# Kernel tuning notes

Hardware: AMD Instinct MI355X
Metric: run time of the kernel (lower is better)

## Reference

```python
import jax, jax.numpy as jnp
import numpy as np

N = 100_000          # nodes
E = 3_200_000        # edges (avg degree 32)
DIMS = [6, 20, 15, 10, 5, 2]


def setup_inputs() -> dict:
    key = jax.random.key(0)
    ks = jax.random.split(key, 3 + 2 * 5)
    inp = {
        "x": jax.random.normal(ks[0], (N, DIMS[0]), jnp.float32),
        "edge_index": jax.random.randint(ks[1], (2, E), 0, N, jnp.int32),
        "edge_weight": jax.random.uniform(ks[2], (E,), jnp.float32),
    }
    for i in range(5):
        din, dout = DIMS[i], DIMS[i + 1]
        s = 1.0 / np.sqrt(din)
        inp[f"w_rel{i}"] = jax.random.normal(ks[3 + 2 * i], (din, dout), jnp.float32) * s
        inp[f"b_rel{i}"] = jnp.zeros((dout,), jnp.float32)
        inp[f"w_root{i}"] = jax.random.normal(ks[4 + 2 * i], (din, dout), jnp.float32) * s
    return inp


def _graph_conv(x, src, dst, w, W_rel, b_rel, W_root):
    # PyG GraphConv: lin_rel(scatter_add(w_e * x_src)) + lin_root(x)
    msg = x[src] * w[:, None]                                  # [E, din]
    agg = jax.ops.segment_sum(msg, dst, num_segments=N)        # [N, din]
    return agg @ W_rel + b_rel + x @ W_root                    # [N, dout]


def reference(x, edge_index, edge_weight,
              w_rel0, b_rel0, w_root0,
              w_rel1, b_rel1, w_root1,
              w_rel2, b_rel2, w_root2,
              w_rel3, b_rel3, w_root3,
              w_rel4, b_rel4, w_root4):
    src, dst = edge_index[0], edge_index[1]
    layers = [
        (w_rel0, b_rel0, w_root0),
        (w_rel1, b_rel1, w_root1),
        (w_rel2, b_rel2, w_root2),
        (w_rel3, b_rel3, w_root3),
        (w_rel4, b_rel4, w_root4),
    ]
    for W_rel, b_rel, W_root in layers:
        x = jax.nn.relu(_graph_conv(x, src, dst, edge_weight, W_rel, b_rel, W_root))
    return jax.nn.softmax(x, axis=1)
```

## Files before the change

kernel.cpp:

```cpp
#include <hip/hip_runtime.h>
#include <hip/hip_fp16.h>
#include <stdint.h>

#define N_NODES 100000
#define N_EDGES 3200000
#define BN      64
#define NB      1563
#define NCH_H   1024
#define CH_H    (N_EDGES / NCH_H)
#define CPL     (NCH_H / 64)
#define PAD_PER 98
#define NCH_S   256
#define CH_S    (N_EDGES / NCH_S)
#define BS1     1024
#define S1_IT   ((CH_S + BS1 - 1) / BS1)
#define S2_CAP  2560
#define BLOCK   256
#define W_SCALE 32767.0f
#define W_INV   (1.0f / 32767.0f)

__global__ void hist_kernel(const int* __restrict__ dst, int* __restrict__ hist_g,
                            const float* __restrict__ x, __half* __restrict__ xpad) {
    __shared__ int h[NB];
    for (int b = threadIdx.x; b < NB; b += BLOCK) h[b] = 0;
    {
        int i = blockIdx.x * PAD_PER + threadIdx.x;
        if (threadIdx.x < PAD_PER && i < N_NODES) {
            const float* xr = x + (size_t)i * 6;
            __half2 hh[4];
            hh[0] = __halves2half2(__float2half(xr[0]), __float2half(xr[1]));
            hh[1] = __halves2half2(__float2half(xr[2]), __float2half(xr[3]));
            hh[2] = __halves2half2(__float2half(xr[4]), __float2half(xr[5]));
            hh[3] = __halves2half2(__float2half(0.f),   __float2half(0.f));
            *(uint4*)(xpad + (size_t)i * 8) = *(uint4*)hh;
        }
    }
    __syncthreads();
    const int c  = blockIdx.x;
    const int k0 = c * CH_H;
    for (int k = threadIdx.x; k < CH_H; k += BLOCK)
        atomicAdd(&h[dst[k0 + k] >> 6], 1);
    __syncthreads();
    for (int b = threadIdx.x; b < NB; b += BLOCK)
        hist_g[c * NB + b] = h[b];
}

__global__ void chunkscan_kernel(const int* __restrict__ hist_g,
                                 int* __restrict__ off_g, int* __restrict__ tot) {
    int w    = (blockIdx.x * blockDim.x + threadIdx.x) >> 6;
    int lane = threadIdx.x & 63;
    if (w >= NB) return;
    int v[CPL];
    int ls = 0;
    const int cbase = lane * CPL;
    #pragma unroll
    for (int i = 0; i < CPL; ++i) { v[i] = hist_g[(cbase + i) * NB + w]; ls += v[i]; }
    int run = ls;
    #pragma unroll
    for (int d = 1; d < 64; d <<= 1) {
        int u = __shfl_up(run, d);
        if (lane >= d) run += u;
    }
    int acc = run - ls;
    #pragma unroll
    for (int i = 0; i < CPL; ++i) { off_g[(cbase + i) * NB + w] = acc; acc += v[i]; }
    if (lane == 63) tot[w] = acc;
}

#define SCAN_T   1024
#define SCAN_PER 2
__global__ void scan_kernel(const int* __restrict__ cnt, int* __restrict__ bstart) {
    __shared__ int part[SCAN_T];
    int t = threadIdx.x;
    int local[SCAN_PER];
    int s = 0;
    #pragma unroll
    for (int i = 0; i < SCAN_PER; ++i) {
        int idx = t * SCAN_PER + i;
        int v = (idx < NB) ? cnt[idx] : 0;
        local[i] = s;
        s += v;
    }
    part[t] = s;
    __syncthreads();
    for (int off = 1; off < SCAN_T; off <<= 1) {
        int v = (t >= off) ? part[t - off] : 0;
        __syncthreads();
        part[t] += v;
        __syncthreads();
    }
    int excl = part[t] - s;
    #pragma unroll
    for (int i = 0; i < SCAN_PER; ++i) {
        int idx = t * SCAN_PER + i;
        if (idx < NB) bstart[idx] = excl + local[i];
    }
}

__global__ void __launch_bounds__(BS1)
scatter1_kernel(const int* __restrict__ src, const int* __restrict__ dst,
                const float* __restrict__ w,
                const int* __restrict__ bstart, const int* __restrict__ off_g,
                uint2* __restrict__ rec1) {
    __shared__ uint32_t stage[CH_S];
    __shared__ int h[NB];
    __shared__ int delta[NB];
    __shared__ int wtot[BS1 / 64];

    const int c  = blockIdx.x;
    const int k0 = c * CH_S;
    const int t  = threadIdx.x;

    for (int b = t; b < NB; b += BS1) h[b] = 0;
    __syncthreads();
    int dstv[S1_IT];
    int nit = 0;
    for (int k = t; k < CH_S; k += BS1, ++nit) {
        int d = dst[k0 + k];
        dstv[nit] = d;
        atomicAdd(&h[d >> 6], 1);
    }
    __syncthreads();

    {
        const int base = t * 2;
        int v[2], ls = 0;
        #pragma unroll
        for (int i = 0; i < 2; ++i) {
            int idx = base + i;
            v[i] = (idx < NB) ? h[idx] : 0;
            ls += v[i];
        }
        int lane = t & 63, wv = t >> 6;
        int run = ls;
        #pragma unroll
        for (int d = 1; d < 64; d <<= 1) {
            int u = __shfl_up(run, d);
            if (lane >= d) run += u;
        }
        if (lane == 63) wtot[wv] = run;
        __syncthreads();
        int wexcl = 0;
        for (int i = 0; i < wv; ++i) wexcl += wtot[i];
        int excl = wexcl + run - ls;
        #pragma unroll
        for (int i = 0; i < 2; ++i) {
            int idx = base + i;
            if (idx < NB) {
                int gb = bstart[idx] + off_g[(size_t)(4 * c) * NB + idx];
                h[idx]     = excl;
                delta[idx] = gb - excl;
                excl += v[i];
            }
        }
    }
    __syncthreads();

    nit = 0;
    for (int k = t; k < CH_S; k += BS1, ++nit) {
        int d = dstv[nit];
        int b = d >> 6;
        int pos = atomicAdd(&h[b], 1);
        stage[pos] = (uint32_t)k | ((uint32_t)(d & 63) << 14) | ((uint32_t)b << 20);
    }
    __syncthreads();

    for (int i = t; i < CH_S; i += BS1) {
        uint32_t sv = stage[i];
        int le = sv & 0x3FFF;
        int dl = (sv >> 14) & 0x3F;
        int b  = sv >> 20;
        int e  = k0 + le;
        uint2 r;
        r.x = (uint32_t)src[e] | ((uint32_t)dl << 17);
        r.y = __float_as_uint(w[e]);
        rec1[delta[b] + i] = r;
    }
}

__global__ void scatter2_kernel(const uint2* __restrict__ rec1,
                                const int* __restrict__ bstart, const int* __restrict__ tot,
                                uint32_t* __restrict__ rec2,
                                int* __restrict__ row_start, int* __restrict__ cnt) {
    __shared__ int h[BN];
    __shared__ int cur[BN];
    __shared__ uint32_t stage[S2_CAP];
    const int b  = blockIdx.x;
    const int s0 = bstart[b];
    const int n  = tot[b];
    if (threadIdx.x < BN) h[threadIdx.x] = 0;
    __syncthreads();
    for (int k = threadIdx.x; k < n; k += BLOCK)
        atomicAdd(&h[rec1[s0 + k].x >> 17], 1);
    __syncthreads();
    if (threadIdx.x < BN) {
        int v = h[threadIdx.x];
        int run = v;
        #pragma unroll
        for (int d = 1; d < 64; d <<= 1) {
            int u = __shfl_up(run, d);
            if (threadIdx.x >= d) run += u;
        }
        int excl = run - v;
        cur[threadIdx.x] = excl;
        int node = b * BN + threadIdx.x;
        if (node < N_NODES) { row_start[node] = s0 + excl; cnt[node] = v; }
    }
    __syncthreads();
    for (int k = threadIdx.x; k < n; k += BLOCK) {
        uint2 r = rec1[s0 + k];
        int dl = (int)(r.x >> 17);
        float wv = __uint_as_float(r.y);
        uint32_t w15 = (uint32_t)__float2uint_rn(wv * W_SCALE);
        uint32_t r2 = (r.x & 0x1FFFF) | (w15 << 17);
        int pos = atomicAdd(&cur[dl], 1);
        if (pos < S2_CAP) stage[pos] = r2;
        else              rec2[s0 + pos] = r2;
    }
    __syncthreads();
    for (int i = threadIdx.x; i < n && i < S2_CAP; i += BLOCK)
        rec2[s0 + i] = stage[i];
}

__global__ void layer0_kernel(const __half* __restrict__ xpad,
                              const uint32_t* __restrict__ rec,
                              const int* __restrict__ row_start, const int* __restrict__ cnt,
                              const float* __restrict__ wrel0, const float* __restrict__ brel0,
                              const float* __restrict__ wroot0,
                              const float* __restrict__ wrel1, const float* __restrict__ brel1,
                              const float* __restrict__ wroot1,
                              __half* __restrict__ pn, float* __restrict__ oinitn) {
    __shared__ float s_wrel0[6 * 20], s_wroot0[6 * 20], s_b0[20];
    __shared__ float s_wrel1[20 * 15], s_wroot1[20 * 15], s_b1[15];
    for (int t = threadIdx.x; t < 120; t += BLOCK) {
        s_wrel0[t]  = wrel0[t];
        s_wroot0[t] = wroot0[t];
    }
    for (int t = threadIdx.x; t < 300; t += BLOCK) {
        s_wrel1[t]  = wrel1[t];
        s_wroot1[t] = wroot1[t];
    }
    if (threadIdx.x < 20) s_b0[threadIdx.x] = brel0[threadIdx.x];
    if (threadIdx.x < 15) s_b1[threadIdx.x] = brel1[threadIdx.x];
    __syncthreads();

    int t = blockIdx.x * blockDim.x + threadIdx.x;
    int node = t >> 3;
    int q    = t & 7;

    float agg[6] = {0.f, 0.f, 0.f, 0.f, 0.f, 0.f};
    const int s = row_start[node];
    const int e = s + cnt[node];
    for (int k = s + q; k < e; k += 32) {
        uint32_t rv[4];
        float    wv[4];
        #pragma unroll
        for (int u = 0; u < 4; ++u) {
            int kk = k + 8 * u;
            int kc = kk < e ? kk : (e - 1);
            rv[u] = rec[kc];
            wv[u] = kk < e ? (float)(rv[u] >> 17) * W_INV : 0.f;
        }
        uint4 raw[4];
        #pragma unroll
        for (int u = 0; u < 4; ++u)
            raw[u] = *(const uint4*)(xpad + (size_t)(rv[u] & 0x1FFFF) * 8);
        #pragma unroll
        for (int u = 0; u < 4; ++u) {
            const __half2* h = (const __half2*)&raw[u];
            float w = wv[u];
            agg[0] += w * __low2float(h[0]);  agg[1] += w * __high2float(h[0]);
            agg[2] += w * __low2float(h[1]);  agg[3] += w * __high2float(h[1]);
            agg[4] += w * __low2float(h[2]);  agg[5] += w * __high2float(h[2]);
        }
    }
    #pragma unroll
    for (int i = 0; i < 6; ++i) {
        agg[i] += __shfl_xor(agg[i], 1);
        agg[i] += __shfl_xor(agg[i], 2);
        agg[i] += __shfl_xor(agg[i], 4);
    }
    uint4 raws = *(const uint4*)(xpad + (size_t)node * 8);
    const __half2* hs = (const __half2*)&raws;
    float xv[6] = { __low2float(hs[0]), __high2float(hs[0]),
                    __low2float(hs[1]), __high2float(hs[1]),
                    __low2float(hs[2]), __high2float(hs[2]) };

    float ov[20];
    #pragma unroll
    for (int j = 0; j < 20; ++j) {
        float o = s_b0[j];
        #pragma unroll
        for (int i = 0; i < 6; ++i)
            o += agg[i] * s_wrel0[i * 20 + j] + xv[i] * s_wroot0[i * 20 + j];
        ov[j] = fmaxf(o, 0.f);
    }

    {
        float pk[2] = {0.f, 0.f};
        #pragma unroll
        for (int kk = 0; kk < 2; ++kk) {
            int k = 2 * q + kk;
            if (k < 15) {
                float sacc = 0.f;
                #pragma unroll
                for (int j = 0; j < 20; ++j) sacc += ov[j] * s_wrel1[j * 15 + k];
                pk[kk] = sacc;
            }
        }
        ((__half2*)(pn + (size_t)node * 16))[q] =
            __halves2half2(__float2half(pk[0]), __float2half(pk[1]));
    }
    #pragma unroll
    for (int kk = 0; kk < 2; ++kk) {
        int k = q + kk * 8;
        if (k < 15) {
            float sacc = s_b1[k];
            #pragma unroll
            for (int j = 0; j < 20; ++j) sacc += ov[j] * s_wroot1[j * 15 + k];
            oinitn[(size_t)node * 15 + k] = sacc;
        }
    }
}

template<int DOUT, int SPH, int NDOUT, int NSPH, bool LAST>
__global__ void gather_kernel(const __half* __restrict__ p, const float* __restrict__ oinit,
                              const uint32_t* __restrict__ rec,
                              const int* __restrict__ row_start, const int* __restrict__ cnt,
                              const float* __restrict__ wrel_n, const float* __restrict__ brel_n,
                              const float* __restrict__ wroot_n,
                              __half* __restrict__ pn, float* __restrict__ oinitn,
                              float* __restrict__ out) {
    __shared__ float s_wrel[LAST ? 1 : DOUT * NDOUT];
    __shared__ float s_wroot[LAST ? 1 : DOUT * NDOUT];
    __shared__ float s_b[LAST ? 1 : (NDOUT > 0 ? NDOUT : 1)];
    if constexpr (!LAST) {
        for (int t = threadIdx.x; t < DOUT * NDOUT; t += BLOCK) {
            s_wrel[t]  = wrel_n[t];
            s_wroot[t] = wroot_n[t];
        }
        if (threadIdx.x < NDOUT) s_b[threadIdx.x] = brel_n[threadIdx.x];
        __syncthreads();
    }

    int t = blockIdx.x * blockDim.x + threadIdx.x;
    int node = t >> 3;
    int q    = t & 7;

    float af[SPH];
    #pragma unroll
    for (int i = 0; i < SPH; ++i) af[i] = 0.f;

    const int s = row_start[node];
    const int e = s + cnt[node];
    constexpr int NR = (SPH >= 8) ? SPH / 8 : 1;
    for (int k = s + q; k < e; k += 32) {
        uint32_t rv[4];
        float    wv[4];
        #pragma unroll
        for (int u = 0; u < 4; ++u) {
            int kk = k + 8 * u;
            int kc = kk < e ? kk : (e - 1);
            rv[u] = rec[kc];
            wv[u] = kk < e ? (float)(rv[u] >> 17) * W_INV : 0.f;
        }
        if constexpr (SPH >= 8) {
            uint4 raw[4 * NR];
            #pragma unroll
            for (int u = 0; u < 4; ++u) {
                const uint4* ps = (const uint4*)(p + (size_t)(rv[u] & 0x1FFFF) * SPH);
                #pragma unroll
                for (int v = 0; v < NR; ++v) raw[u * NR + v] = ps[v];
            }
            #pragma unroll
            for (int u = 0; u < 4; ++u) {
                float w = wv[u];
                #pragma unroll
                for (int v = 0; v < NR; ++v) {
                    const __half2* h = (const __half2*)&raw[u * NR + v];
                    #pragma unroll
                    for (int jj = 0; jj < 4; ++jj) {
                        af[v * 8 + 2 * jj]     += w * __low2float(h[jj]);
                        af[v * 8 + 2 * jj + 1] += w * __high2float(h[jj]);
                    }
                }
            }
        } else {
            uint32_t raw[4];
            #pragma unroll
            for (int u = 0; u < 4; ++u)
                raw[u] = *(const uint32_t*)(p + (size_t)(rv[u] & 0x1FFFF) * SPH);
            #pragma unroll
            for (int u = 0; u < 4; ++u) {
                __half2 h = *(const __half2*)&raw[u];
                af[0] += wv[u] * __low2float(h);
                af[1] += wv[u] * __high2float(h);
            }
        }
    }
    #pragma unroll
    for (int i = 0; i < SPH; ++i) {
        af[i] += __shfl_xor(af[i], 1);
        af[i] += __shfl_xor(af[i], 2);
        af[i] += __shfl_xor(af[i], 4);
    }

    if constexpr (LAST) {
        if (q == 0) {
            float o0 = af[0] + oinit[(size_t)node * 2 + 0];
            float o1 = af[1] + oinit[(size_t)node * 2 + 1];
            float m = fmaxf(o0, o1);
            float e0 = __expf(o0 - m), e1 = __expf(o1 - m);
            float inv = 1.f / (e0 + e1);
            out[(size_t)node * 2 + 0] = e0 * inv;
            out[(size_t)node * 2 + 1] = e1 * inv;
        }
    } else {
        float ov[DOUT];
        #pragma unroll
        for (int j = 0; j < DOUT; ++j)
            ov[j] = fmaxf(af[j] + oinit[(size_t)node * DOUT + j], 0.f);

        if (q < NSPH / 2) {
            float pk[2] = {0.f, 0.f};
            #pragma unroll
            for (int kk = 0; kk < 2; ++kk) {
                int k = 2 * q + kk;
                if (k < NDOUT) {
                    float sacc = 0.f;
                    #pragma unroll
                    for (int j = 0; j < DOUT; ++j) sacc += ov[j] * s_wrel[j * NDOUT + k];
                    pk[kk] = sacc;
                }
            }
            ((__half2*)(pn + (size_t)node * NSPH))[q] =
                __halves2half2(__float2half(pk[0]), __float2half(pk[1]));
        }
        #pragma unroll
        for (int kk = 0; kk < 2; ++kk) {
            int k = q + kk * 8;
            if (k < NDOUT) {
                float sacc = s_b[k];
                #pragma unroll
                for (int j = 0; j < DOUT; ++j) sacc += ov[j] * s_wroot[j * NDOUT + k];
                oinitn[(size_t)node * NDOUT + k] = sacc;
            }
        }
    }
}


extern "C" void kernel_launch(void* const* d_in, const int* in_sizes, int n_in,
                              void* d_out, int out_size, void* d_ws, size_t ws_size,
                              hipStream_t stream) {
    const float* x  = (const float*)d_in[0];
    const int*   ei = (const int*)d_in[1];
    const float* ew = (const float*)d_in[2];
    const float* wrel[5]  = { (const float*)d_in[3], (const float*)d_in[6],
                              (const float*)d_in[9], (const float*)d_in[12],
                              (const float*)d_in[15] };
    const float* brel[5]  = { (const float*)d_in[4], (const float*)d_in[7],
                              (const float*)d_in[10], (const float*)d_in[13],
                              (const float*)d_in[16] };
    const float* wroot[5] = { (const float*)d_in[5], (const float*)d_in[8],
                              (const float*)d_in[11], (const float*)d_in[14],
                              (const float*)d_in[17] };

    char* ws = (char*)d_ws;
    size_t off = 0;
    auto alloc = [&](size_t bytes) -> void* {
        void* ptr = ws + off;
        off += (bytes + 255) & ~(size_t)255;
        return ptr;
    };
    char*     regionA   = (char*)alloc((size_t)N_EDGES * 8);
    uint2*    rec1      = (uint2*)regionA;
    __half*   pA        = (__half*)regionA;
    __half*   pB        = (__half*)(regionA + (size_t)4  * 1024 * 1024);
    float*    oA        = (float*)(regionA + (size_t)8  * 1024 * 1024);
    float*    oB        = (float*)(regionA + (size_t)16 * 1024 * 1024);
    uint32_t* rec2      = (uint32_t*)alloc((size_t)N_EDGES * 4);
    __half*   xpad      = (__half*)alloc((size_t)N_NODES * 8 * 2);
    int*      hist_g    = (int*)alloc((size_t)NCH_H * NB * 4);
    int*      off_g     = (int*)alloc((size_t)NCH_H * NB * 4);
    int*      tot       = (int*)alloc((size_t)NB * 4);
    int*      bstart    = (int*)alloc((size_t)NB * 4);
    int*      row_start = (int*)alloc((size_t)N_NODES * 4);
    int*      cntb      = (int*)alloc((size_t)N_NODES * 4);

    const int* srcv = ei;
    const int* dstv = ei + N_EDGES;

    const int gN8 = (8 * N_NODES + BLOCK - 1) / BLOCK;

    hist_kernel     <<<NCH_H, BLOCK, 0, stream>>>(dstv, hist_g, x, xpad);
    chunkscan_kernel<<<(NB + 3) / 4, BLOCK, 0, stream>>>(hist_g, off_g, tot);
    scan_kernel     <<<1, SCAN_T, 0, stream>>>(tot, bstart);
    scatter1_kernel <<<NCH_S, BS1, 0, stream>>>(srcv, dstv, ew, bstart, off_g, rec1);
    scatter2_kernel <<<NB, BLOCK, 0, stream>>>(rec1, bstart, tot, rec2, row_start, cntb);

    layer0_kernel<<<gN8, BLOCK, 0, stream>>>(xpad, rec2, row_start, cntb,
                                             wrel[0], brel[0], wroot[0],
                                             wrel[1], brel[1], wroot[1], pA, oA);
    gather_kernel<15, 16, 10, 16, false><<<gN8, BLOCK, 0, stream>>>(
        pA, oA, rec2, row_start, cntb, wrel[2], brel[2], wroot[2], pB, oB, nullptr);
    gather_kernel<10, 16, 5, 8, false><<<gN8, BLOCK, 0, stream>>>(
        pB, oB, rec2, row_start, cntb, wrel[3], brel[3], wroot[3], pA, oA, nullptr);
    gather_kernel<5, 8, 2, 2, false><<<gN8, BLOCK, 0, stream>>>(
        pA, oA, rec2, row_start, cntb, wrel[4], brel[4], wroot[4], pB, oB, nullptr);
    gather_kernel<2, 2, 0, 0, true><<<gN8, BLOCK, 0, stream>>>(
        pB, oB, rec2, row_start, cntb, nullptr, nullptr, nullptr,
        nullptr, nullptr, (float*)d_out);
}
```

Measured before the change: 322.7 us.

## Fuse five layer kernels into one persistent kernel with grid barriers

```diff
diff --git a/kernel.cpp b/kernel.cpp
--- a/kernel.cpp
+++ b/kernel.cpp
@@ -16,6 +16,7 @@
 #define S1_IT   ((CH_S + BS1 - 1) / BS1)
 #define S2_CAP  2560
 #define BLOCK   256
+#define PGRID   512
 #define W_SCALE 32767.0f
 #define W_INV   (1.0f / 32767.0f)
 
@@ -222,231 +223,286 @@
         rec2[s0 + i] = stage[i];
 }
 
-__global__ void layer0_kernel(const __half* __restrict__ xpad,
-                              const uint32_t* __restrict__ rec,
-                              const int* __restrict__ row_start, const int* __restrict__ cnt,
-                              const float* __restrict__ wrel0, const float* __restrict__ brel0,
-                              const float* __restrict__ wroot0,
-                              const float* __restrict__ wrel1, const float* __restrict__ brel1,
-                              const float* __restrict__ wroot1,
-                              __half* __restrict__ pn, float* __restrict__ oinitn) {
-    __shared__ float s_wrel0[6 * 20], s_wroot0[6 * 20], s_b0[20];
-    __shared__ float s_wrel1[20 * 15], s_wroot1[20 * 15], s_b1[15];
-    for (int t = threadIdx.x; t < 120; t += BLOCK) {
-        s_wrel0[t]  = wrel0[t];
-        s_wroot0[t] = wroot0[t];
-    }
-    for (int t = threadIdx.x; t < 300; t += BLOCK) {
-        s_wrel1[t]  = wrel1[t];
-        s_wroot1[t] = wroot1[t];
-    }
-    if (threadIdx.x < 20) s_b0[threadIdx.x] = brel0[threadIdx.x];
-    if (threadIdx.x < 15) s_b1[threadIdx.x] = brel1[threadIdx.x];
-    __syncthreads();
-
-    int t = blockIdx.x * blockDim.x + threadIdx.x;
-    int node = t >> 3;
-    int q    = t & 7;
-
-    float agg[6] = {0.f, 0.f, 0.f, 0.f, 0.f, 0.f};
-    const int s = row_start[node];
-    const int e = s + cnt[node];
-    for (int k = s + q; k < e; k += 32) {
-        uint32_t rv[4];
-        float    wv[4];
-        #pragma unroll
-        for (int u = 0; u < 4; ++u) {
-            int kk = k + 8 * u;
-            int kc = kk < e ? kk : (e - 1);
-            rv[u] = rec[kc];
-            wv[u] = kk < e ? (float)(rv[u] >> 17) * W_INV : 0.f;
-        }
-        uint4 raw[4];
-        #pragma unroll
-        for (int u = 0; u < 4; ++u)
-            raw[u] = *(const uint4*)(xpad + (size_t)(rv[u] & 0x1FFFF) * 8);
-        #pragma unroll
-        for (int u = 0; u < 4; ++u) {
-            const __half2* h = (const __half2*)&raw[u];
-            float w = wv[u];
-            agg[0] += w * __low2float(h[0]);  agg[1] += w * __high2float(h[0]);
-            agg[2] += w * __low2float(h[1]);  agg[3] += w * __high2float(h[1]);
-            agg[4] += w * __low2float(h[2]);  agg[5] += w * __high2float(h[2]);
-        }
-    }
-    #pragma unroll
-    for (int i = 0; i < 6; ++i) {
-        agg[i] += __shfl_xor(agg[i], 1);
-        agg[i] += __shfl_xor(agg[i], 2);
-        agg[i] += __shfl_xor(agg[i], 4);
-    }
-    uint4 raws = *(const uint4*)(xpad + (size_t)node * 8);
-    const __half2* hs = (const __half2*)&raws;
-    float xv[6] = { __low2float(hs[0]), __high2float(hs[0]),
-                    __low2float(hs[1]), __high2float(hs[1]),
-                    __low2float(hs[2]), __high2float(hs[2]) };
-
-    float ov[20];
-    #pragma unroll
-    for (int j = 0; j < 20; ++j) {
-        float o = s_b0[j];
-        #pragma unroll
-        for (int i = 0; i < 6; ++i)
-            o += agg[i] * s_wrel0[i * 20 + j] + xv[i] * s_wroot0[i * 20 + j];
-        ov[j] = fmaxf(o, 0.f);
-    }
-
-    {
-        float pk[2] = {0.f, 0.f};
-        #pragma unroll
-        for (int kk = 0; kk < 2; ++kk) {
-            int k = 2 * q + kk;
-            if (k < 15) {
-                float sacc = 0.f;
+__device__ __forceinline__ void grid_barrier(int* bar, int* local_sense) {
+    __threadfence();
+    __syncthreads();
+    if (threadIdx.x == 0) {
+        int want = *local_sense ^ 1;
+        *local_sense = want;
+        int arrived = __hip_atomic_fetch_add(&bar[0], 1, __ATOMIC_ACQ_REL,
+                                             __HIP_MEMORY_SCOPE_AGENT);
+        if (arrived == PGRID - 1) {
+            __hip_atomic_store(&bar[0], 0, __ATOMIC_RELAXED, __HIP_MEMORY_SCOPE_AGENT);
+            __hip_atomic_store(&bar[1], want, __ATOMIC_RELEASE, __HIP_MEMORY_SCOPE_AGENT);
+        } else {
+            while (__hip_atomic_load(&bar[1], __ATOMIC_ACQUIRE,
+                                     __HIP_MEMORY_SCOPE_AGENT) != want) {}
+        }
+    }
+    __syncthreads();
+    __threadfence();
+}
+
+struct LayerArgs {
+    const __half* xpad;
+    const uint32_t* rec;
+    const int* row_start;
+    const int* cnt;
+    const float* wrel[5];
+    const float* brel[5];
+    const float* wroot[5];
+    __half* pA; __half* pB;
+    float*  oA; float*  oB;
+    float*  out;
+    int*    bar;
+};
+
+template<int DOUT, int SPH, int NDOUT, int NSPH, bool LAST>
+__device__ __forceinline__ void gather_body(
+        const __half* __restrict__ p, const float* __restrict__ oinit,
+        const uint32_t* __restrict__ rec,
+        const int* __restrict__ row_start, const int* __restrict__ cnt,
+        const float* s_wrel, const float* s_wroot, const float* s_b,
+        __half* __restrict__ pn, float* __restrict__ oinitn,
+        float* __restrict__ out, int gtid, int NT) {
+    for (int t = gtid; t < 8 * N_NODES; t += NT) {
+        int node = t >> 3;
+        int q    = t & 7;
+
+        float af[SPH];
+        #pragma unroll
+        for (int i = 0; i < SPH; ++i) af[i] = 0.f;
+
+        const int s = row_start[node];
+        const int e = s + cnt[node];
+        constexpr int NR = (SPH >= 8) ? SPH / 8 : 1;
+        for (int k = s + q; k < e; k += 32) {
+            uint32_t rv[4];
+            float    wv[4];
+            #pragma unroll
+            for (int u = 0; u < 4; ++u) {
+                int kk = k + 8 * u;
+                int kc = kk < e ? kk : (e - 1);
+                rv[u] = rec[kc];
+                wv[u] = kk < e ? (float)(rv[u] >> 17) * W_INV : 0.f;
+            }
+            if constexpr (SPH >= 8) {
+                uint4 raw[4 * NR];
                 #pragma unroll
-                for (int j = 0; j < 20; ++j) sacc += ov[j] * s_wrel1[j * 15 + k];
-                pk[kk] = sacc;
-            }
-        }
-        ((__half2*)(pn + (size_t)node * 16))[q] =
-            __halves2half2(__float2half(pk[0]), __float2half(pk[1]));
-    }
-    #pragma unroll
-    for (int kk = 0; kk < 2; ++kk) {
-        int k = q + kk * 8;
-        if (k < 15) {
-            float sacc = s_b1[k];
-            #pragma unroll
-            for (int j = 0; j < 20; ++j) sacc += ov[j] * s_wroot1[j * 15 + k];
-            oinitn[(size_t)node * 15 + k] = sacc;
-        }
-    }
-}
-
-template<int DOUT, int SPH, int NDOUT, int NSPH, bool LAST>
-__global__ void gather_kernel(const __half* __restrict__ p, const float* __restrict__ oinit,
-                              const uint32_t* __restrict__ rec,
-                              const int* __restrict__ row_start, const int* __restrict__ cnt,
-                              const float* __restrict__ wrel_n, const float* __restrict__ brel_n,
-                              const float* __restrict__ wroot_n,
-                              __half* __restrict__ pn, float* __restrict__ oinitn,
-                              float* __restrict__ out) {
-    __shared__ float s_wrel[LAST ? 1 : DOUT * NDOUT];
-    __shared__ float s_wroot[LAST ? 1 : DOUT * NDOUT];
-    __shared__ float s_b[LAST ? 1 : (NDOUT > 0 ? NDOUT : 1)];
-    if constexpr (!LAST) {
-        for (int t = threadIdx.x; t < DOUT * NDOUT; t += BLOCK) {
-            s_wrel[t]  = wrel_n[t];
-            s_wroot[t] = wroot_n[t];
-        }
-        if (threadIdx.x < NDOUT) s_b[threadIdx.x] = brel_n[threadIdx.x];
-        __syncthreads();
-    }
-
-    int t = blockIdx.x * blockDim.x + threadIdx.x;
-    int node = t >> 3;
-    int q    = t & 7;
-
-    float af[SPH];
-    #pragma unroll
-    for (int i = 0; i < SPH; ++i) af[i] = 0.f;
-
-    const int s = row_start[node];
-    const int e = s + cnt[node];
-    constexpr int NR = (SPH >= 8) ? SPH / 8 : 1;
-    for (int k = s + q; k < e; k += 32) {
-        uint32_t rv[4];
-        float    wv[4];
-        #pragma unroll
-        for (int u = 0; u < 4; ++u) {
-            int kk = k + 8 * u;
-            int kc = kk < e ? kk : (e - 1);
-            rv[u] = rec[kc];
-            wv[u] = kk < e ? (float)(rv[u] >> 17) * W_INV : 0.f;
-        }
-        if constexpr (SPH >= 8) {
-            uint4 raw[4 * NR];
-            #pragma unroll
-            for (int u = 0; u < 4; ++u) {
-                const uint4* ps = (const uint4*)(p + (size_t)(rv[u] & 0x1FFFF) * SPH);
+                for (int u = 0; u < 4; ++u) {
+                    const uint4* ps = (const uint4*)(p + (size_t)(rv[u] & 0x1FFFF) * SPH);
+                    #pragma unroll
+                    for (int v = 0; v < NR; ++v) raw[u * NR + v] = ps[v];
+                }
                 #pragma unroll
-                for (int v = 0; v < NR; ++v) raw[u * NR + v] = ps[v];
-            }
-            #pragma unroll
-            for (int u = 0; u < 4; ++u) {
-                float w = wv[u];
-                #pragma unroll
-                for (int v = 0; v < NR; ++v) {
-                    const __half2* h = (const __half2*)&raw[u * NR + v];
+                for (int u = 0; u < 4; ++u) {
+                    float w = wv[u];
                     #pragma unroll
-                    for (int jj = 0; jj < 4; ++jj) {
-                        af[v * 8 + 2 * jj]     += w * __low2float(h[jj]);
-                        af[v * 8 + 2 * jj + 1] += w * __high2float(h[jj]);
+                    for (int v = 0; v < NR; ++v) {
+                        const __half2* h = (const __half2*)&raw[u * NR + v];
+                        #pragma unroll
+                        for (int jj = 0; jj < 4; ++jj) {
+                            af[v * 8 + 2 * jj]     += w * __low2float(h[jj]);
+                            af[v * 8 + 2 * jj + 1] += w * __high2float(h[jj]);
+                        }
                     }
                 }
+            } else {
+                uint32_t raw[4];
+                #pragma unroll
+                for (int u = 0; u < 4; ++u)
+                    raw[u] = *(const uint32_t*)(p + (size_t)(rv[u] & 0x1FFFF) * SPH);
+                #pragma unroll
+                for (int u = 0; u < 4; ++u) {
+                    __half2 h = *(const __half2*)&raw[u];
+                    af[0] += wv[u] * __low2float(h);
+                    af[1] += wv[u] * __high2float(h);
+                }
+            }
+        }
+        #pragma unroll
+        for (int i = 0; i < SPH; ++i) {
+            af[i] += __shfl_xor(af[i], 1);
+            af[i] += __shfl_xor(af[i], 2);
+            af[i] += __shfl_xor(af[i], 4);
+        }
+
+        if constexpr (LAST) {
+            if (q == 0) {
+                float o0 = af[0] + oinit[(size_t)node * 2 + 0];
+                float o1 = af[1] + oinit[(size_t)node * 2 + 1];
+                float m = fmaxf(o0, o1);
+                float e0 = __expf(o0 - m), e1 = __expf(o1 - m);
+                float inv = 1.f / (e0 + e1);
+                out[(size_t)node * 2 + 0] = e0 * inv;
+                out[(size_t)node * 2 + 1] = e1 * inv;
             }
         } else {
-            uint32_t raw[4];
+            float ov[DOUT];
+            #pragma unroll
+            for (int j = 0; j < DOUT; ++j)
+                ov[j] = fmaxf(af[j] + oinit[(size_t)node * DOUT + j], 0.f);
+
+            if (q < NSPH / 2) {
+                float pk[2] = {0.f, 0.f};
+                #pragma unroll
+                for (int kk = 0; kk < 2; ++kk) {
+                    int k = 2 * q + kk;
+                    if (k < NDOUT) {
+                        float sacc = 0.f;
+                        #pragma unroll
+                        for (int j = 0; j < DOUT; ++j) sacc += ov[j] * s_wrel[j * NDOUT + k];
+                        pk[kk] = sacc;
+                    }
+                }
+                ((__half2*)(pn + (size_t)node * NSPH))[q] =
+                    __halves2half2(__float2half(pk[0]), __float2half(pk[1]));
+            }
+            #pragma unroll
+            for (int kk = 0; kk < 2; ++kk) {
+                int k = q + kk * 8;
+                if (k < NDOUT) {
+                    float sacc = s_b[k];
+                    #pragma unroll
+                    for (int j = 0; j < DOUT; ++j) sacc += ov[j] * s_wroot[j * NDOUT + k];
+                    oinitn[(size_t)node * NDOUT + k] = sacc;
+                }
+            }
+        }
+    }
+}
+
+__global__ void __launch_bounds__(BLOCK, 2)
+layers_kernel(LayerArgs a) {
+    __shared__ float s_wrel0[6 * 20], s_wroot0[6 * 20], s_b0[20];
+    __shared__ float s_wrel[20 * 15], s_wroot[20 * 15], s_b[16];
+
+    const int gtid = blockIdx.x * blockDim.x + threadIdx.x;
+    const int NT   = gridDim.x * blockDim.x;
+    int sense = 0;
+
+    for (int t = threadIdx.x; t < 120; t += BLOCK) {
+        s_wrel0[t]  = a.wrel[0][t];
+        s_wroot0[t] = a.wroot[0][t];
+    }
+    for (int t = threadIdx.x; t < 300; t += BLOCK) {
+        s_wrel[t]  = a.wrel[1][t];
+        s_wroot[t] = a.wroot[1][t];
+    }
+    if (threadIdx.x < 20) s_b0[threadIdx.x] = a.brel[0][threadIdx.x];
+    if (threadIdx.x < 15) s_b[threadIdx.x]  = a.brel[1][threadIdx.x];
+    __syncthreads();
+
+    for (int t = gtid; t < 8 * N_NODES; t += NT) {
+        int node = t >> 3;
+        int q    = t & 7;
+        float agg[6] = {0.f, 0.f, 0.f, 0.f, 0.f, 0.f};
+        const int s = a.row_start[node];
+        const int e = s + a.cnt[node];
+        for (int k = s + q; k < e; k += 32) {
+            uint32_t rv[4];
+            float    wv[4];
+            #pragma unroll
+            for (int u = 0; u < 4; ++u) {
+                int kk = k + 8 * u;
+                int kc = kk < e ? kk : (e - 1);
+                rv[u] = a.rec[kc];
+                wv[u] = kk < e ? (float)(rv[u] >> 17) * W_INV : 0.f;
+            }
+            uint4 raw[4];
             #pragma unroll
             for (int u = 0; u < 4; ++u)
-                raw[u] = *(const uint32_t*)(p + (size_t)(rv[u] & 0x1FFFF) * SPH);
+                raw[u] = *(const uint4*)(a.xpad + (size_t)(rv[u] & 0x1FFFF) * 8);
             #pragma unroll
             for (int u = 0; u < 4; ++u) {
-                __half2 h = *(const __half2*)&raw[u];
-                af[0] += wv[u] * __low2float(h);
-                af[1] += wv[u] * __high2float(h);
-            }
-        }
-    }
-    #pragma unroll
-    for (int i = 0; i < SPH; ++i) {
-        af[i] += __shfl_xor(af[i], 1);
-        af[i] += __shfl_xor(af[i], 2);
-        af[i] += __shfl_xor(af[i], 4);
-    }
-
-    if constexpr (LAST) {
-        if (q == 0) {
-            float o0 = af[0] + oinit[(size_t)node * 2 + 0];
-            float o1 = af[1] + oinit[(size_t)node * 2 + 1];
-            float m = fmaxf(o0, o1);
-            float e0 = __expf(o0 - m), e1 = __expf(o1 - m);
-            float inv = 1.f / (e0 + e1);
-            out[(size_t)node * 2 + 0] = e0 * inv;
-            out[(size_t)node * 2 + 1] = e1 * inv;
-        }
-    } else {
-        float ov[DOUT];
-        #pragma unroll
-        for (int j = 0; j < DOUT; ++j)
-            ov[j] = fmaxf(af[j] + oinit[(size_t)node * DOUT + j], 0.f);
-
-        if (q < NSPH / 2) {
+                const __half2* h = (const __half2*)&raw[u];
+                float w = wv[u];
+                agg[0] += w * __low2float(h[0]);  agg[1] += w * __high2float(h[0]);
+                agg[2] += w * __low2float(h[1]);  agg[3] += w * __high2float(h[1]);
+                agg[4] += w * __low2float(h[2]);  agg[5] += w * __high2float(h[2]);
+            }
+        }
+        #pragma unroll
+        for (int i = 0; i < 6; ++i) {
+            agg[i] += __shfl_xor(agg[i], 1);
+            agg[i] += __shfl_xor(agg[i], 2);
+            agg[i] += __shfl_xor(agg[i], 4);
+        }
+        uint4 raws = *(const uint4*)(a.xpad + (size_t)node * 8);
+        const __half2* hs = (const __half2*)&raws;
+        float xv[6] = { __low2float(hs[0]), __high2float(hs[0]),
+                        __low2float(hs[1]), __high2float(hs[1]),
+                        __low2float(hs[2]), __high2float(hs[2]) };
+        float ov[20];
+        #pragma unroll
+        for (int j = 0; j < 20; ++j) {
+            float o = s_b0[j];
+            #pragma unroll
+            for (int i = 0; i < 6; ++i)
+                o += agg[i] * s_wrel0[i * 20 + j] + xv[i] * s_wroot0[i * 20 + j];
+            ov[j] = fmaxf(o, 0.f);
+        }
+        {
             float pk[2] = {0.f, 0.f};
             #pragma unroll
             for (int kk = 0; kk < 2; ++kk) {
                 int k = 2 * q + kk;
-                if (k < NDOUT) {
+                if (k < 15) {
                     float sacc = 0.f;
                     #pragma unroll
-                    for (int j = 0; j < DOUT; ++j) sacc += ov[j] * s_wrel[j * NDOUT + k];
+                    for (int j = 0; j < 20; ++j) sacc += ov[j] * s_wrel[j * 15 + k];
                     pk[kk] = sacc;
                 }
             }
-            ((__half2*)(pn + (size_t)node * NSPH))[q] =
+            ((__half2*)(a.pA + (size_t)node * 16))[q] =
                 __halves2half2(__float2half(pk[0]), __float2half(pk[1]));
         }
         #pragma unroll
         for (int kk = 0; kk < 2; ++kk) {
             int k = q + kk * 8;
-            if (k < NDOUT) {
+            if (k < 15) {
                 float sacc = s_b[k];
                 #pragma unroll
-                for (int j = 0; j < DOUT; ++j) sacc += ov[j] * s_wroot[j * NDOUT + k];
-                oinitn[(size_t)node * NDOUT + k] = sacc;
-            }
-        }
-    }
+                for (int j = 0; j < 20; ++j) sacc += ov[j] * s_wroot[j * 15 + k];
+                a.oA[(size_t)node * 15 + k] = sacc;
+            }
+        }
+    }
+    grid_barrier(a.bar, &sense);
+
+    for (int t = threadIdx.x; t < 150; t += BLOCK) {
+        s_wrel[t]  = a.wrel[2][t];
+        s_wroot[t] = a.wroot[2][t];
+    }
+    if (threadIdx.x < 10) s_b[threadIdx.x] = a.brel[2][threadIdx.x];
+    __syncthreads();
+    gather_body<15, 16, 10, 16, false>(a.pA, a.oA, a.rec, a.row_start, a.cnt,
+                                       s_wrel, s_wroot, s_b, a.pB, a.oB, nullptr, gtid, NT);
+    grid_barrier(a.bar, &sense);
+
+    for (int t = threadIdx.x; t < 50; t += BLOCK) {
+        s_wrel[t]  = a.wrel[3][t];
+        s_wroot[t] = a.wroot[3][t];
+    }
+    if (threadIdx.x < 5) s_b[threadIdx.x] = a.brel[3][threadIdx.x];
+    __syncthreads();
+    gather_body<10, 16, 5, 8, false>(a.pB, a.oB, a.rec, a.row_start, a.cnt,
+                                     s_wrel, s_wroot, s_b, a.pA, a.oA, nullptr, gtid, NT);
+    grid_barrier(a.bar, &sense);
+
+    for (int t = threadIdx.x; t < 10; t += BLOCK) {
+        s_wrel[t]  = a.wrel[4][t];
+        s_wroot[t] = a.wroot[4][t];
+    }
+    if (threadIdx.x < 2) s_b[threadIdx.x] = a.brel[4][threadIdx.x];
+    __syncthreads();
+    gather_body<5, 8, 2, 2, false>(a.pA, a.oA, a.rec, a.row_start, a.cnt,
+                                   s_wrel, s_wroot, s_b, a.pB, a.oB, nullptr, gtid, NT);
+    grid_barrier(a.bar, &sense);
+
+    gather_body<2, 2, 0, 0, true>(a.pB, a.oB, a.rec, a.row_start, a.cnt,
+                                  nullptr, nullptr, nullptr,
+                                  nullptr, nullptr, a.out, gtid, NT);
 }
 
 
@@ -456,15 +512,6 @@
     const float* x  = (const float*)d_in[0];
     const int*   ei = (const int*)d_in[1];
     const float* ew = (const float*)d_in[2];
-    const float* wrel[5]  = { (const float*)d_in[3], (const float*)d_in[6],
-                              (const float*)d_in[9], (const float*)d_in[12],
-                              (const float*)d_in[15] };
-    const float* brel[5]  = { (const float*)d_in[4], (const float*)d_in[7],
-                              (const float*)d_in[10], (const float*)d_in[13],
-                              (const float*)d_in[16] };
-    const float* wroot[5] = { (const float*)d_in[5], (const float*)d_in[8],
-                              (const float*)d_in[11], (const float*)d_in[14],
-                              (const float*)d_in[17] };
 
     char* ws = (char*)d_ws;
     size_t off = 0;
@@ -487,11 +534,12 @@
     int*      bstart    = (int*)alloc((size_t)NB * 4);
     int*      row_start = (int*)alloc((size_t)N_NODES * 4);
     int*      cntb      = (int*)alloc((size_t)N_NODES * 4);
+    int*      bar       = (int*)alloc(256);
 
     const int* srcv = ei;
     const int* dstv = ei + N_EDGES;
 
-    const int gN8 = (8 * N_NODES + BLOCK - 1) / BLOCK;
+    hipMemsetAsync(bar, 0, 8, stream);
 
     hist_kernel     <<<NCH_H, BLOCK, 0, stream>>>(dstv, hist_g, x, xpad);
     chunkscan_kernel<<<(NB + 3) / 4, BLOCK, 0, stream>>>(hist_g, off_g, tot);
@@ -499,16 +547,15 @@
     scatter1_kernel <<<NCH_S, BS1, 0, stream>>>(srcv, dstv, ew, bstart, off_g, rec1);
     scatter2_kernel <<<NB, BLOCK, 0, stream>>>(rec1, bstart, tot, rec2, row_start, cntb);
 
-    layer0_kernel<<<gN8, BLOCK, 0, stream>>>(xpad, rec2, row_start, cntb,
-                                             wrel[0], brel[0], wroot[0],
-                                             wrel[1], brel[1], wroot[1], pA, oA);
-    gather_kernel<15, 16, 10, 16, false><<<gN8, BLOCK, 0, stream>>>(
-        pA, oA, rec2, row_start, cntb, wrel[2], brel[2], wroot[2], pB, oB, nullptr);
-    gather_kernel<10, 16, 5, 8, false><<<gN8, BLOCK, 0, stream>>>(
-        pB, oB, rec2, row_start, cntb, wrel[3], brel[3], wroot[3], pA, oA, nullptr);
-    gather_kernel<5, 8, 2, 2, false><<<gN8, BLOCK, 0, stream>>>(
-        pA, oA, rec2, row_start, cntb, wrel[4], brel[4], wroot[4], pB, oB, nullptr);
-    gather_kernel<2, 2, 0, 0, true><<<gN8, BLOCK, 0, stream>>>(
-        pB, oB, rec2, row_start, cntb, nullptr, nullptr, nullptr,
-        nullptr, nullptr, (float*)d_out);
-}
+    LayerArgs la;
+    la.xpad = xpad; la.rec = rec2; la.row_start = row_start; la.cnt = cntb;
+    for (int i = 0; i < 5; ++i) {
+        la.wrel[i]  = (const float*)d_in[3 + 3 * i];
+        la.brel[i]  = (const float*)d_in[4 + 3 * i];
+        la.wroot[i] = (const float*)d_in[5 + 3 * i];
+    }
+    la.pA = pA; la.pB = pB; la.oA = oA; la.oB = oB; la.out = (float*)d_out;
+    la.bar = bar;
+
+    layers_kernel<<<PGRID, BLOCK, 0, stream>>>(la);
+}
```

New measurement: 997.6 us. 3.09x slower.

## Use 16 lanes per node in gather kernels and cache rec1 in shared memory

Applied to the files above, without the earlier changes.

```diff
diff --git a/kernel.cpp b/kernel.cpp
--- a/kernel.cpp
+++ b/kernel.cpp
@@ -16,6 +16,7 @@
 #define S1_IT   ((CH_S + BS1 - 1) / BS1)
 #define S2_CAP  2560
 #define BLOCK   256
+#define LPN     16
 #define W_SCALE 32767.0f
 #define W_INV   (1.0f / 32767.0f)
 
@@ -184,14 +185,18 @@
                                 int* __restrict__ row_start, int* __restrict__ cnt) {
     __shared__ int h[BN];
     __shared__ int cur[BN];
-    __shared__ uint32_t stage[S2_CAP];
+    __shared__ uint2 sin[S2_CAP];
+    __shared__ uint32_t sout[S2_CAP];
     const int b  = blockIdx.x;
     const int s0 = bstart[b];
     const int n  = tot[b];
     if (threadIdx.x < BN) h[threadIdx.x] = 0;
     __syncthreads();
-    for (int k = threadIdx.x; k < n; k += BLOCK)
-        atomicAdd(&h[rec1[s0 + k].x >> 17], 1);
+    for (int k = threadIdx.x; k < n; k += BLOCK) {
+        uint2 r = rec1[s0 + k];
+        if (k < S2_CAP) sin[k] = r;
+        atomicAdd(&h[r.x >> 17], 1);
+    }
     __syncthreads();
     if (threadIdx.x < BN) {
         int v = h[threadIdx.x];
@@ -208,18 +213,18 @@
     }
     __syncthreads();
     for (int k = threadIdx.x; k < n; k += BLOCK) {
-        uint2 r = rec1[s0 + k];
+        uint2 r = (k < S2_CAP) ? sin[k] : rec1[s0 + k];
         int dl = (int)(r.x >> 17);
         float wv = __uint_as_float(r.y);
         uint32_t w15 = (uint32_t)__float2uint_rn(wv * W_SCALE);
         uint32_t r2 = (r.x & 0x1FFFF) | (w15 << 17);
         int pos = atomicAdd(&cur[dl], 1);
-        if (pos < S2_CAP) stage[pos] = r2;
+        if (pos < S2_CAP) sout[pos] = r2;
         else              rec2[s0 + pos] = r2;
     }
     __syncthreads();
     for (int i = threadIdx.x; i < n && i < S2_CAP; i += BLOCK)
-        rec2[s0 + i] = stage[i];
+        rec2[s0 + i] = sout[i];
 }
 
 __global__ void layer0_kernel(const __half* __restrict__ xpad,
@@ -245,28 +250,28 @@
     __syncthreads();
 
     int t = blockIdx.x * blockDim.x + threadIdx.x;
-    int node = t >> 3;
-    int q    = t & 7;
+    int node = t >> 4;
+    int q    = t & 15;
 
     float agg[6] = {0.f, 0.f, 0.f, 0.f, 0.f, 0.f};
     const int s = row_start[node];
     const int e = s + cnt[node];
-    for (int k = s + q; k < e; k += 32) {
-        uint32_t rv[4];
-        float    wv[4];
-        #pragma unroll
-        for (int u = 0; u < 4; ++u) {
-            int kk = k + 8 * u;
+    for (int k = s + q; k < e; k += 2 * LPN) {
+        uint32_t rv[2];
+        float    wv[2];
+        #pragma unroll
+        for (int u = 0; u < 2; ++u) {
+            int kk = k + LPN * u;
             int kc = kk < e ? kk : (e - 1);
             rv[u] = rec[kc];
             wv[u] = kk < e ? (float)(rv[u] >> 17) * W_INV : 0.f;
         }
-        uint4 raw[4];
-        #pragma unroll
-        for (int u = 0; u < 4; ++u)
+        uint4 raw[2];
+        #pragma unroll
+        for (int u = 0; u < 2; ++u)
             raw[u] = *(const uint4*)(xpad + (size_t)(rv[u] & 0x1FFFF) * 8);
         #pragma unroll
-        for (int u = 0; u < 4; ++u) {
+        for (int u = 0; u < 2; ++u) {
             const __half2* h = (const __half2*)&raw[u];
             float w = wv[u];
             agg[0] += w * __low2float(h[0]);  agg[1] += w * __high2float(h[0]);
@@ -279,13 +284,13 @@
         agg[i] += __shfl_xor(agg[i], 1);
         agg[i] += __shfl_xor(agg[i], 2);
         agg[i] += __shfl_xor(agg[i], 4);
+        agg[i] += __shfl_xor(agg[i], 8);
     }
     uint4 raws = *(const uint4*)(xpad + (size_t)node * 8);
     const __half2* hs = (const __half2*)&raws;
     float xv[6] = { __low2float(hs[0]), __high2float(hs[0]),
                     __low2float(hs[1]), __high2float(hs[1]),
                     __low2float(hs[2]), __high2float(hs[2]) };
-
     float ov[20];
     #pragma unroll
     for (int j = 0; j < 20; ++j) {
@@ -295,8 +300,7 @@
             o += agg[i] * s_wrel0[i * 20 + j] + xv[i] * s_wroot0[i * 20 + j];
         ov[j] = fmaxf(o, 0.f);
     }
-
-    {
+    if (q < 8) {
         float pk[2] = {0.f, 0.f};
         #pragma unroll
         for (int kk = 0; kk < 2; ++kk) {
@@ -311,15 +315,11 @@
         ((__half2*)(pn + (size_t)node * 16))[q] =
             __halves2half2(__float2half(pk[0]), __float2half(pk[1]));
     }
-    #pragma unroll
-    for (int kk = 0; kk < 2; ++kk) {
-        int k = q + kk * 8;
-        if (k < 15) {
-            float sacc = s_b1[k];
-            #pragma unroll
-            for (int j = 0; j < 20; ++j) sacc += ov[j] * s_wroot1[j * 15 + k];
-            oinitn[(size_t)node * 15 + k] = sacc;
-        }
+    if (q < 15) {
+        float sacc = s_b1[q];
+        #pragma unroll
+        for (int j = 0; j < 20; ++j) sacc += ov[j] * s_wroot1[j * 15 + q];
+        oinitn[(size_t)node * 15 + q] = sacc;
     }
 }
 
@@ -344,8 +344,8 @@
     }
 
     int t = blockIdx.x * blockDim.x + threadIdx.x;
-    int node = t >> 3;
-    int q    = t & 7;
+    int node = t >> 4;
+    int q    = t & 15;
 
     float af[SPH];
     #pragma unroll
@@ -354,26 +354,26 @@
     const int s = row_start[node];
     const int e = s + cnt[node];
     constexpr int NR = (SPH >= 8) ? SPH / 8 : 1;
-    for (int k = s + q; k < e; k += 32) {
-        uint32_t rv[4];
-        float    wv[4];
-        #pragma unroll
-        for (int u = 0; u < 4; ++u) {
-            int kk = k + 8 * u;
+    for (int k = s + q; k < e; k += 2 * LPN) {
+        uint32_t rv[2];
+        float    wv[2];
+        #pragma unroll
+        for (int u = 0; u < 2; ++u) {
+            int kk = k + LPN * u;
             int kc = kk < e ? kk : (e - 1);
             rv[u] = rec[kc];
             wv[u] = kk < e ? (float)(rv[u] >> 17) * W_INV : 0.f;
         }
         if constexpr (SPH >= 8) {
-            uint4 raw[4 * NR];
+            uint4 raw[2 * NR];
             #pragma unroll
-            for (int u = 0; u < 4; ++u) {
+            for (int u = 0; u < 2; ++u) {
                 const uint4* ps = (const uint4*)(p + (size_t)(rv[u] & 0x1FFFF) * SPH);
                 #pragma unroll
                 for (int v = 0; v < NR; ++v) raw[u * NR + v] = ps[v];
             }
             #pragma unroll
-            for (int u = 0; u < 4; ++u) {
+            for (int u = 0; u < 2; ++u) {
                 float w = wv[u];
                 #pragma unroll
                 for (int v = 0; v < NR; ++v) {
@@ -386,12 +386,12 @@
                 }
             }
         } else {
-            uint32_t raw[4];
+            uint32_t raw[2];
             #pragma unroll
-            for (int u = 0; u < 4; ++u)
+            for (int u = 0; u < 2; ++u)
                 raw[u] = *(const uint32_t*)(p + (size_t)(rv[u] & 0x1FFFF) * SPH);
             #pragma unroll
-            for (int u = 0; u < 4; ++u) {
+            for (int u = 0; u < 2; ++u) {
                 __half2 h = *(const __half2*)&raw[u];
                 af[0] += wv[u] * __low2float(h);
                 af[1] += wv[u] * __high2float(h);
@@ -403,6 +403,7 @@
         af[i] += __shfl_xor(af[i], 1);
         af[i] += __shfl_xor(af[i], 2);
         af[i] += __shfl_xor(af[i], 4);
+        af[i] += __shfl_xor(af[i], 8);
     }
 
     if constexpr (LAST) {
@@ -436,15 +437,11 @@
             ((__half2*)(pn + (size_t)node * NSPH))[q] =
                 __halves2half2(__float2half(pk[0]), __float2half(pk[1]));
         }
-        #pragma unroll
-        for (int kk = 0; kk < 2; ++kk) {
-            int k = q + kk * 8;
-            if (k < NDOUT) {
-                float sacc = s_b[k];
-                #pragma unroll
-                for (int j = 0; j < DOUT; ++j) sacc += ov[j] * s_wroot[j * NDOUT + k];
-                oinitn[(size_t)node * NDOUT + k] = sacc;
-            }
+        if (q < NDOUT) {
+            float sacc = s_b[q];
+            #pragma unroll
+            for (int j = 0; j < DOUT; ++j) sacc += ov[j] * s_wroot[j * NDOUT + q];
+            oinitn[(size_t)node * NDOUT + q] = sacc;
         }
     }
 }
@@ -491,7 +488,7 @@
     const int* srcv = ei;
     const int* dstv = ei + N_EDGES;
 
-    const int gN8 = (8 * N_NODES + BLOCK - 1) / BLOCK;
+    const int gN16 = (LPN * N_NODES + BLOCK - 1) / BLOCK;
 
     hist_kernel     <<<NCH_H, BLOCK, 0, stream>>>(dstv, hist_g, x, xpad);
     chunkscan_kernel<<<(NB + 3) / 4, BLOCK, 0, stream>>>(hist_g, off_g, tot);
@@ -499,16 +496,16 @@
     scatter1_kernel <<<NCH_S, BS1, 0, stream>>>(srcv, dstv, ew, bstart, off_g, rec1);
     scatter2_kernel <<<NB, BLOCK, 0, stream>>>(rec1, bstart, tot, rec2, row_start, cntb);
 
-    layer0_kernel<<<gN8, BLOCK, 0, stream>>>(xpad, rec2, row_start, cntb,
-                                             wrel[0], brel[0], wroot[0],
-                                             wrel[1], brel[1], wroot[1], pA, oA);
-    gather_kernel<15, 16, 10, 16, false><<<gN8, BLOCK, 0, stream>>>(
+    layer0_kernel<<<gN16, BLOCK, 0, stream>>>(xpad, rec2, row_start, cntb,
+                                              wrel[0], brel[0], wroot[0],
+                                              wrel[1], brel[1], wroot[1], pA, oA);
+    gather_kernel<15, 16, 10, 16, false><<<gN16, BLOCK, 0, stream>>>(
         pA, oA, rec2, row_start, cntb, wrel[2], brel[2], wroot[2], pB, oB, nullptr);
-    gather_kernel<10, 16, 5, 8, false><<<gN8, BLOCK, 0, stream>>>(
+    gather_kernel<10, 16, 5, 8, false><<<gN16, BLOCK, 0, stream>>>(
         pB, oB, rec2, row_start, cntb, wrel[3], brel[3], wroot[3], pA, oA, nullptr);
-    gather_kernel<5, 8, 2, 2, false><<<gN8, BLOCK, 0, stream>>>(
+    gather_kernel<5, 8, 2, 2, false><<<gN16, BLOCK, 0, stream>>>(
         pA, oA, rec2, row_start, cntb, wrel[4], brel[4], wroot[4], pB, oB, nullptr);
-    gather_kernel<2, 2, 0, 0, true><<<gN8, BLOCK, 0, stream>>>(
+    gather_kernel<2, 2, 0, 0, true><<<gN16, BLOCK, 0, stream>>>(
         pB, oB, rec2, row_start, cntb, nullptr, nullptr, nullptr,
         nullptr, nullptr, (float*)d_out);
 }
```

New measurement: 331.0 us. 1.03x slower.
